# Optimization experiments

Hardware: AMD Instinct MI355X
Metric: run time of the kernel (lower is better)

## Reference

```python
import jax, jax.numpy as jnp
import numpy as np

K = 5        # spline kernel_size per dim (dim=2 -> 25 kernel weights)
NPG = 75     # MNIST superpixel nodes per graph


def _spline_conv(x, src, dst, pseudo, emask, W, root, bias):
    """SplineConv, dim=2, kernel_size=5, degree=1 open splines, aggr='mean'.
    emask in {0,1} masks out coalesced-away (duplicate/self-loop) edges."""
    n = x.shape[0]
    v = jnp.clip(pseudo, 0.0, 1.0) * (K - 1)
    bot = jnp.clip(jnp.floor(v), 0, K - 2)
    frac = v - bot                                   # [E,2]
    bot = bot.astype(jnp.int32)
    xj = x[src] * emask[:, None]                     # [E,Fin] gathered source feats
    # aggregate-then-transform: acc[k,i,:] = sum over edges into i with basis k
    acc = jnp.zeros((K * K, n, x.shape[1]), x.dtype)
    for o0 in (0, 1):
        for o1 in (0, 1):
            w = (frac[:, 0] if o0 else 1.0 - frac[:, 0]) * (frac[:, 1] if o1 else 1.0 - frac[:, 1])
            kk = (bot[:, 0] + o0) + K * (bot[:, 1] + o1)
            acc = acc.at[kk, dst].add(w[:, None] * xj)
    out = jnp.einsum('knf,kfo->no', acc, W)
    deg = jax.ops.segment_sum(emask, dst, num_segments=n)
    return out / jnp.maximum(deg, 1.0)[:, None] + x @ root + bias


def _pool(x, pos, valid, batch, src, dst, emask, size, G, B):
    """voxel_grid + max_pool with static shapes: S=B*G*G clusters, masked."""
    S = B * G * G
    c = jnp.clip(jnp.floor(pos / size).astype(jnp.int32), 0, G - 1)
    cl = batch * (G * G) + c[:, 1] * G + c[:, 0]
    xm = jnp.where(valid[:, None] > 0, x, -1e30)
    px = jax.ops.segment_max(xm, cl, num_segments=S)
    cnt = jax.ops.segment_sum(valid, cl, num_segments=S)
    sval = (cnt > 0).astype(x.dtype)
    px = jnp.where(sval[:, None] > 0, px, 0.0)
    ppos = jax.ops.segment_sum(pos * valid[:, None], cl, num_segments=S) / jnp.maximum(cnt, 1.0)[:, None]
    nb = jnp.arange(S, dtype=jnp.int32) // (G * G)
    # remap edges to clusters; mask self loops and duplicates (= coalesce)
    nsrc, ndst = cl[src], cl[dst]
    m = (emask > 0) & (nsrc != ndst)
    a0 = jnp.where(m, nsrc, S)
    b0 = jnp.where(m, ndst, S)
    order = jnp.lexsort((b0, a0))
    a, b = a0[order], b0[order]
    first = jnp.concatenate([jnp.array([True]), (a[1:] != a[:-1]) | (b[1:] != b[:-1])])
    keep = jnp.zeros(src.shape[0], dtype=bool).at[order].set(first & (a < S))
    kf = keep.astype(x.dtype)
    # T.Cartesian(cat=False, norm=True): pseudo = (pos_src-pos_dst)/(2*max|.|)+0.5
    cart = ppos[nsrc] - ppos[ndst]
    amax = jnp.maximum(jnp.max(jnp.abs(cart) * kf[:, None]), 1e-12)
    pseudo = cart / (2.0 * amax) + 0.5
    return px, ppos, sval, nb, nsrc, ndst, kf, pseudo


def _forward(x, pos, src, dst, W1, r1, b1, W2, r2, b2, W3, r3, b3, fw1, fb1, fw2, fb2):
    N = x.shape[0]
    B = N // NPG
    batch = jnp.arange(N, dtype=jnp.int32) // NPG
    valid = jnp.ones((N,), x.dtype)
    emask = jnp.ones((src.shape[0],), x.dtype)
    cart = pos[src] - pos[dst]
    pseudo = cart / (2.0 * jnp.maximum(jnp.max(jnp.abs(cart)), 1e-12)) + 0.5
    x = jax.nn.elu(_spline_conv(x, src, dst, pseudo, emask, W1, r1, b1))
    x, pos, valid, batch, src, dst, emask, pseudo = _pool(x, pos, valid, batch, src, dst, emask, 5.0, 6, B)
    x = jax.nn.elu(_spline_conv(x, src, dst, pseudo, emask, W2, r2, b2))
    x, pos, valid, batch, src, dst, emask, pseudo = _pool(x, pos, valid, batch, src, dst, emask, 7.0, 5, B)
    x = jax.nn.elu(_spline_conv(x, src, dst, pseudo, emask, W3, r3, b3))
    # max_pool_x(cluster, x, batch, size=4): 2x2 voxel grid (size=14, end=27.99)
    c = jnp.clip(jnp.floor(pos / 14.0).astype(jnp.int32), 0, 1)
    cl = batch * 4 + c[:, 1] * 2 + c[:, 0]
    xm = jnp.where(valid[:, None] > 0, x, -1e30)
    px = jax.ops.segment_max(xm, cl, num_segments=B * 4)
    cnt = jax.ops.segment_sum(valid, cl, num_segments=B * 4)
    px = jnp.where((cnt > 0)[:, None], px, 0.0)
    h = jax.nn.elu(px.reshape(B, 4 * 64) @ fw1.T + fb1)
    logits = h @ fw2.T + fb2  # F.dropout is identity in eval mode
    return jax.nn.log_softmax(logits, axis=1)


def setup_inputs() -> dict:
    key = jax.random.key(0)
    ks = jax.random.split(key, 16)
    B, EPG = 1024, 1392
    N = B * NPG
    x = jax.random.normal(ks[0], (N, 1), jnp.float32)
    pos = jax.random.uniform(ks[1], (N, 2), jnp.float32) * 27.99
    s = jax.random.randint(ks[2], (B, EPG), 0, NPG)
    d = (s + 1 + jax.random.randint(ks[3], (B, EPG), 0, NPG - 1)) % NPG  # no self loops
    off = (jnp.arange(B, dtype=jnp.int32) * NPG)[:, None]
    src = (s + off).reshape(-1)
    dst = (d + off).reshape(-1)
    rn = lambda k, sh, sc: jax.random.normal(k, sh, jnp.float32) * sc
    return dict(x=x, pos=pos, src=src, dst=dst,
                W1=rn(ks[4], (25, 1, 32), 0.2), r1=rn(ks[5], (1, 32), 0.2), b1=jnp.zeros((32,), jnp.float32),
                W2=rn(ks[6], (25, 32, 64), 0.05), r2=rn(ks[7], (32, 64), 0.1), b2=jnp.zeros((64,), jnp.float32),
                W3=rn(ks[8], (25, 64, 64), 0.04), r3=rn(ks[9], (64, 64), 0.08), b3=jnp.zeros((64,), jnp.float32),
                fw1=rn(ks[10], (128, 256), 0.06), fb1=jnp.zeros((128,), jnp.float32),
                fw2=rn(ks[11], (10, 128), 0.09), fb2=jnp.zeros((10,), jnp.float32))


def reference(x, pos, src, dst, W1, r1, b1, W2, r2, b2, W3, r3, b3, fw1, fb1, fw2, fb2):
    return _forward(x, pos, src, dst, W1, r1, b1, W2, r2, b2, W3, r3, b3, fw1, fb1, fw2, fb2)
```

## Files before the change

kernel.cpp:

```cpp
#include <hip/hip_runtime.h>
#include <math.h>

#define NPG 75
#define KDIM 5

typedef _Float16 half8 __attribute__((ext_vector_type(8)));
typedef _Float16 half4 __attribute__((ext_vector_type(4)));
typedef float f32x4 __attribute__((ext_vector_type(4)));

__device__ __forceinline__ float eluf(float v){ return v > 0.f ? v : expf(v) - 1.f; }

__device__ __forceinline__ unsigned fenc(float f){
    unsigned u = __float_as_uint(f);
    return (u & 0x80000000u) ? ~u : (u | 0x80000000u);
}
__device__ __forceinline__ float fdec(unsigned u){
    return (u & 0x80000000u) ? __uint_as_float(u & 0x7FFFFFFFu) : __uint_as_float(~u);
}

__device__ __forceinline__ void fma25(float (&r)[25], const float (&wx)[5], const float (&wyx)[5]){
    #pragma unroll
    for (int b1 = 0; b1 < 5; b1++)
        #pragma unroll
        for (int b0 = 0; b0 < 5; b0++)
            asm("v_fmac_f32 %0, %1, %2" : "+v"(r[b1 * 5 + b0]) : "v"(wx[b0]), "v"(wyx[b1]));
}

__device__ __forceinline__ void spline2(float c0, float c1, float am, int* kks, float* wsp){
    float denom = 2.f * fmaxf(am, 1e-12f);
    float p0 = c0 / denom + 0.5f;
    float p1 = c1 / denom + 0.5f;
    p0 = fminf(fmaxf(p0, 0.f), 1.f) * 4.f;
    p1 = fminf(fmaxf(p1, 0.f), 1.f) * 4.f;
    float b0 = fminf(floorf(p0), 3.f);
    float b1 = fminf(floorf(p1), 3.f);
    float f0 = p0 - b0, f1 = p1 - b1;
    int i0 = (int)b0, i1 = (int)b1;
    wsp[0] = (1.f - f0) * (1.f - f1); kks[0] = i0     + KDIM *  i1;
    wsp[1] =        f0  * (1.f - f1); kks[1] = i0 + 1 + KDIM *  i1;
    wsp[2] = (1.f - f0) *        f1 ; kks[2] = i0     + KDIM * (i1 + 1);
    wsp[3] =        f0  *        f1 ; kks[3] = i0 + 1 + KDIM * (i1 + 1);
}

__global__ __launch_bounds__(256) void amax0_k(
        const float* __restrict__ pos, const int* __restrict__ src,
        const int* __restrict__ dst, int E4, float* __restrict__ pbmax){
    int i = blockIdx.x * 256 + threadIdx.x;
    float cand = 0.f;
    if (i < E4){
        int4 s4 = ((const int4*)src)[i];
        int4 d4 = ((const int4*)dst)[i];
        #pragma unroll
        for (int k = 0; k < 4; k++){
            int s = (&s4.x)[k], d = (&d4.x)[k];
            float c0 = pos[s*2]   - pos[d*2];
            float c1 = pos[s*2+1] - pos[d*2+1];
            cand = fmaxf(cand, fmaxf(fabsf(c0), fabsf(c1)));
        }
    }
    __shared__ float sm[256];
    sm[threadIdx.x] = cand; __syncthreads();
    for (int o = 128; o > 0; o >>= 1){
        if (threadIdx.x < o) sm[threadIdx.x] = fmaxf(sm[threadIdx.x], sm[threadIdx.x + o]);
        __syncthreads();
    }
    if (threadIdx.x == 0) pbmax[blockIdx.x] = sm[0];
}

__global__ __launch_bounds__(1024) void reduce_max_k(const float* __restrict__ pbmax, int n,
                                                     unsigned* __restrict__ outbits){
    __shared__ float sm[1024];
    float cand = 0.f;
    for (int i = threadIdx.x; i < n; i += 1024) cand = fmaxf(cand, pbmax[i]);
    sm[threadIdx.x] = cand; __syncthreads();
    for (int o = 512; o > 0; o >>= 1){
        if (threadIdx.x < o) sm[threadIdx.x] = fmaxf(sm[threadIdx.x], sm[threadIdx.x + o]);
        __syncthreads();
    }
    if (threadIdx.x == 0) *outbits = __float_as_uint(sm[0]);
}

__global__ __launch_bounds__(512) void conv1pool1_k(
        const float* __restrict__ x, const float* __restrict__ pos,
        const int* __restrict__ src, const int* __restrict__ dst, int EPG,
        const unsigned* __restrict__ amaxp,
        const float* __restrict__ W1, const float* __restrict__ r1, const float* __restrict__ b1,
        float* __restrict__ px1, float* __restrict__ pp1, float* __restrict__ sv1,
        int* __restrict__ cl1){
    __shared__ float acc[NPG * 25];
    __shared__ float deg[NPG];
    __shared__ float xl[NPG], p0l[NPG], p1l[NPG];
    __shared__ int   cli[NPG];
    __shared__ float W1s[800], r1s[32], b1s[32];
    __shared__ unsigned px[36 * 32];
    __shared__ float cnt[36], ps[72];

    const int b = blockIdx.x, t = threadIdx.x;
    const int n0 = b * NPG, e0 = b * EPG;

    for (int i = t; i < NPG * 25; i += 512) acc[i] = 0.f;
    for (int i = t; i < 36 * 32; i += 512) px[i] = 0u;
    if (t < NPG) deg[t] = 0.f;
    if (t < 36) cnt[t] = 0.f;
    if (t < 72) ps[t] = 0.f;
    for (int i = t; i < 800; i += 512) W1s[i] = W1[i];
    if (t < 32){ r1s[t] = r1[t]; b1s[t] = b1[t]; }
    if (t < NPG){
        float p0 = pos[(n0 + t) * 2], p1 = pos[(n0 + t) * 2 + 1];
        xl[t] = x[n0 + t]; p0l[t] = p0; p1l[t] = p1;
        int c0 = min(max((int)floorf(p0 / 5.f), 0), 5);
        int c1 = min(max((int)floorf(p1 / 5.f), 0), 5);
        int c = c1 * 6 + c0;
        cli[t] = c;
        cl1[n0 + t] = b * 36 + c;
    }
    __syncthreads();
    if (t < NPG){
        int c = cli[t];
        atomicAdd(&cnt[c], 1.f);
        atomicAdd(&ps[c*2],     p0l[t]);
        atomicAdd(&ps[c*2 + 1], p1l[t]);
    }

    const float am = __uint_as_float(*amaxp);
    for (int e = t; e < EPG; e += 512){
        int s = src[e0 + e] - n0;
        int d = dst[e0 + e] - n0;
        float c0 = p0l[s] - p0l[d];
        float c1 = p1l[s] - p1l[d];
        int kks[4]; float wsp[4];
        spline2(c0, c1, am, kks, wsp);
        float xv = xl[s];
        #pragma unroll
        for (int c = 0; c < 4; c++) atomicAdd(&acc[d*25 + kks[c]], wsp[c] * xv);
        atomicAdd(&deg[d], 1.f);
    }
    __syncthreads();

    for (int idx = t; idx < NPG * 32; idx += 512){
        int i = idx >> 5, o = idx & 31;
        float sum = 0.f;
        #pragma unroll
        for (int k = 0; k < 25; k++) sum += acc[i*25 + k] * W1s[k*32 + o];
        float v = sum / fmaxf(deg[i], 1.f) + xl[i] * r1s[o] + b1s[o];
        v = eluf(v);
        atomicMax(&px[cli[i]*32 + o], fenc(v));
    }
    __syncthreads();

    for (int idx = t; idx < 36 * 32; idx += 512){
        int s_ = idx >> 5;
        float c = cnt[s_];
        px1[(size_t)(b*36)*32 + idx] = (c > 0.f) ? fdec(px[idx]) : 0.f;
    }
    if (t < 36){
        float c = cnt[t], m = fmaxf(c, 1.f);
        pp1[(b*36 + t)*2]     = ps[t*2] / m;
        pp1[(b*36 + t)*2 + 1] = ps[t*2 + 1] / m;
        sv1[b*36 + t] = (c > 0.f) ? 1.f : 0.f;
    }
}

template<int GG, int NN>
__global__ __launch_bounds__(1024) void dedup_csr_k(
        const int* src_in, const int* dst_in,
        const int* __restrict__ clmap, const unsigned char* __restrict__ kf_in,
        unsigned char* kf_out, int* es_out, int* ed_out,
        const float* __restrict__ pp, int EPG,
        int* __restrict__ easrc, float2* __restrict__ ecart,
        int* __restrict__ rowptr2, int* __restrict__ kcnt, float* __restrict__ pbmax){
    __shared__ unsigned pm[GG * GG];
    __shared__ float degs[GG];
    __shared__ int rs[GG + 1];
    __shared__ int cur[GG];
    __shared__ float red[16];
    __shared__ int   clS[NN];
    __shared__ float ppS[2 * GG];

    const int b = blockIdx.x, t = threadIdx.x;
    const int lane = t & 63, wid = t >> 6;
    const int e0 = b * EPG;
    const int cbase = b * GG;

    for (int i = t; i < GG * GG; i += 1024) pm[i] = 0xFFFFFFFFu;
    if (t < GG) degs[t] = 0.f;
    if (t < NN) clS[t] = clmap[b * NN + t] - cbase;
    if (t < 2 * GG) ppS[t] = pp[cbase * 2 + t];
    __syncthreads();

    const int niter = (EPG + 1023) / 1024;
    int la[2], lb[2]; bool lm[2];
    const int nbase = b * NN;
    for (int it = 0; it < niter; it++){
        int e = t + it * 1024;
        lm[it] = false;
        if (e < EPG){
            int a  = clS[src_in[e0 + e] - nbase];
            int bb = clS[dst_in[e0 + e] - nbase];
            la[it] = a; lb[it] = bb;
            es_out[e0 + e] = cbase + a; ed_out[e0 + e] = cbase + bb;
            bool m = (kf_in ? (kf_in[e0 + e] != 0) : true) && (a != bb);
            lm[it] = m;
            if (m) atomicMin(&pm[a * GG + bb], (unsigned)e);
        }
    }
    __syncthreads();

    float cand = 0.f;
    bool kept[2]; float lc0[2], lc1[2];
    for (int it = 0; it < niter; it++){
        int e = t + it * 1024;
        kept[it] = false;
        if (e < EPG){
            bool k = false;
            if (lm[it]) k = (pm[la[it] * GG + lb[it]] == (unsigned)e);
            kept[it] = k;
            if (kf_out) kf_out[e0 + e] = k ? 1 : 0;
            if (k){
                atomicAdd(&degs[lb[it]], 1.f);
                float c0 = ppS[la[it]*2]     - ppS[lb[it]*2];
                float c1 = ppS[la[it]*2 + 1] - ppS[lb[it]*2 + 1];
                lc0[it] = c0; lc1[it] = c1;
                cand = fmaxf(cand, fmaxf(fabsf(c0), fabsf(c1)));
            }
        }
    }
    #pragma unroll
    for (int o = 1; o < 64; o <<= 1) cand = fmaxf(cand, __shfl_xor(cand, o, 64));
    if (lane == 0) red[wid] = cand;
    __syncthreads();
    if (t == 0){
        float m = red[0];
        #pragma unroll
        for (int i = 1; i < 16; i++) m = fmaxf(m, red[i]);
        pbmax[b] = m;
    }
    if (t < 64){
        int v = (t < GG) ? (int)degs[t] : 0;
        int incl = v;
        #pragma unroll
        for (int o = 1; o < 64; o <<= 1){
            int u = __shfl_up(incl, o, 64);
            if (t >= o) incl += u;
        }
        if (t == 0) rs[0] = 0;
        if (t < GG) rs[t + 1] = incl;
    }
    __syncthreads();
    if (t < GG){
        rowptr2[(cbase + t)*2]     = e0 + rs[t];
        rowptr2[(cbase + t)*2 + 1] = e0 + rs[t + 1];
        cur[t] = rs[t];
    }
    if (t == 0) kcnt[b] = rs[GG];
    __syncthreads();
    for (int it = 0; it < niter; it++){
        if (kept[it]){
            int slot = atomicAdd(&cur[lb[it]], 1);
            easrc[e0 + slot] = cbase + la[it];
            ecart[e0 + slot] = make_float2(lc0[it], lc1[it]);
        }
    }
}

__global__ void espline_k(const float2* __restrict__ ecart, const unsigned* __restrict__ amaxp,
                          const int* __restrict__ kcnt, int EPG, int E,
                          float* __restrict__ edata){
    int i = blockIdx.x * 256 + threadIdx.x;
    if (i >= E) return;
    int b = i / EPG;
    if (i - b * EPG >= kcnt[b]) return;
    float2 c = ecart[i];
    float am = __uint_as_float(*amaxp);
    float denom = 2.f * fmaxf(am, 1e-12f);
    float p0 = fminf(fmaxf(c.x / denom + 0.5f, 0.f), 1.f) * 4.f;
    float p1 = fminf(fmaxf(c.y / denom + 0.5f, 0.f), 1.f) * 4.f;
    float b0 = fminf(floorf(p0), 3.f);
    float b1 = fminf(floorf(p1), 3.f);
    int i0 = (int)b0, i1 = (int)b1;
    float f0 = p0 - b0, f1 = p1 - b1;
    float wx[5], wy[5];
    #pragma unroll
    for (int k = 0; k < 5; k++){
        wx[k] = (k == i0) ? (1.f - f0) : ((k == i0 + 1) ? f0 : 0.f);
        wy[k] = (k == i1) ? (1.f - f1) : ((k == i1 + 1) ? f1 : 0.f);
    }
    float* d = edata + (size_t)i * 8;
    *(float4*)(d)     = make_float4(wx[0], wx[1], wx[2], wx[3]);
    *(float4*)(d + 4) = make_float4(wy[0], wy[1], wy[2], wy[3]);
}

template<int CIN, int G>
__global__ __launch_bounds__(256) void pool_mid_k(
        const float* __restrict__ xin, const float* __restrict__ ppin,
        const float* __restrict__ svin, float size,
        float* __restrict__ pxout, float* __restrict__ ppout, float* __restrict__ svout,
        int* __restrict__ clout){
    __shared__ unsigned px[G * G * 64];
    __shared__ float cnt[G * G], ps[2 * G * G];
    __shared__ int cli[CIN];
    const int b = blockIdx.x, t = threadIdx.x;

    for (int i = t; i < G * G * 64; i += 256) px[i] = 0u;
    if (t < G * G){ cnt[t] = 0.f; ps[t*2] = 0.f; ps[t*2 + 1] = 0.f; }
    if (t < CIN){
        float v  = svin[b*CIN + t];
        float p0 = ppin[(b*CIN + t)*2], p1 = ppin[(b*CIN + t)*2 + 1];
        int c0 = min(max((int)floorf(p0 / size), 0), G - 1);
        int c1 = min(max((int)floorf(p1 / size), 0), G - 1);
        int c = c1 * G + c0;
        cli[t] = (v > 0.f) ? c : -1;
        clout[b*CIN + t] = b * G * G + c;
    }
    __syncthreads();
    if (t < CIN && cli[t] >= 0){
        int c = cli[t];
        atomicAdd(&cnt[c], 1.f);
        atomicAdd(&ps[c*2],     ppin[(b*CIN + t)*2]);
        atomicAdd(&ps[c*2 + 1], ppin[(b*CIN + t)*2 + 1]);
    }
    __syncthreads();
    for (int idx = t; idx < CIN * 64; idx += 256){
        int i = idx >> 6, f = idx & 63;
        if (cli[i] >= 0)
            atomicMax(&px[cli[i]*64 + f], fenc(xin[(size_t)(b*CIN + i)*64 + f]));
    }
    __syncthreads();
    for (int idx = t; idx < G * G * 64; idx += 256){
        int s_ = idx >> 6;
        pxout[(size_t)(b*G*G)*64 + idx] = (cnt[s_] > 0.f) ? fdec(px[idx]) : 0.f;
    }
    if (t < G * G){
        float c = cnt[t], m = fmaxf(c, 1.f);
        ppout[(b*G*G + t)*2]     = ps[t*2] / m;
        ppout[(b*G*G + t)*2 + 1] = ps[t*2 + 1] / m;
        svout[b*G*G + t] = (c > 0.f) ? 1.f : 0.f;
    }
}

__global__ void wswz_k(const float* __restrict__ W, const float* __restrict__ root,
                       int FIN, _Float16* __restrict__ Wz){
    int gid = blockIdx.x * 256 + threadIdx.x;
    int KT = 26 * FIN;
    if (gid >= KT * 64) return;
    int k = gid >> 6, n = gid & 63;
    float v = (k < 25 * FIN) ? W[(size_t)k * 64 + n] : root[(size_t)(k - 25 * FIN) * 64 + n];
    int kt = k >> 5, kr = k & 31, quad = kr >> 3, j = kr & 7;
    int lane = (quad << 4) | (n & 15);
    int nt = n >> 4;
    Wz[(((size_t)(kt * 4 + nt) * 64 + lane) << 3) + j] = (_Float16)v;
}

template<int FIN>
__global__ __launch_bounds__(64) void conv_gather_k(
        const float* __restrict__ x, const int* __restrict__ easrc,
        const float* __restrict__ edata,
        const int* __restrict__ rowptr2, int n, _Float16* __restrict__ Aout){
    constexpr int KTOT = 26 * FIN;
    const int lane = threadIdx.x;
    const int node = blockIdx.x;
    const int row0 = rowptr2[node*2], row1 = rowptr2[node*2 + 1];
    constexpr int STEP = (FIN == 32) ? 2 : 1;
    const int sub = (FIN == 32) ? (lane >> 5) : 0;
    const int f = lane & (FIN - 1);

    float r[25];
    #pragma unroll
    for (int b = 0; b < 25; b++) r[b] = 0.f;

    int iCur = row0 + sub;
    int aNext = 0;
    float4 waC, wbC;
    float xvCur = 0.f;
    if (iCur < row1){
        int aCur = easrc[iCur];
        const float* d = edata + (size_t)iCur * 8;
        waC = *(const float4*)(d); wbC = *(const float4*)(d + 4);
        xvCur = x[(size_t)aCur * FIN + f];
        int i1 = (iCur + STEP < row1) ? iCur + STEP : iCur;
        aNext = easrc[i1];
    }
    for (; iCur < row1; iCur += STEP){
        int iN  = iCur + STEP;
        int iNs = (iN < row1) ? iN : iCur;
        int iN2 = (iN + STEP < row1) ? iN + STEP : iNs;
        const float* dn = edata + (size_t)iNs * 8;
        float4 waN = *(const float4*)(dn);
        float4 wbN = *(const float4*)(dn + 4);
        float xvN = x[(size_t)aNext * FIN + f];
        int aN2 = easrc[iN2];
        float wx4 = 1.f - (waC.x + waC.y + waC.z + waC.w);
        float wy4 = 1.f - (wbC.x + wbC.y + wbC.z + wbC.w);
        float wx[5]  = {waC.x, waC.y, waC.z, waC.w, wx4};
        float wyx[5] = {wbC.x * xvCur, wbC.y * xvCur, wbC.z * xvCur, wbC.w * xvCur, wy4 * xvCur};
        fma25(r, wx, wyx);
        waC = waN; wbC = wbN; xvCur = xvN; aNext = aN2;
    }

    if (FIN == 32){
        #pragma unroll
        for (int b = 0; b < 25; b++) r[b] += __shfl_xor(r[b], 32, 64);
    }

    float inv = 1.f / (float)max(row1 - row0, 1);
    _Float16* dstrow = Aout + (size_t)node * KTOT;
    if (FIN == 64){
        #pragma unroll
        for (int b = 0; b < 25; b++) dstrow[b * 64 + f] = (_Float16)(r[b] * inv);
        dstrow[25 * 64 + f] = (_Float16)x[(size_t)node * 64 + f];
    } else {
        #pragma unroll
        for (int b = 0; b < 25; b++)
            if ((b & 1) == sub) dstrow[b * 32 + f] = (_Float16)(r[b] * inv);
        if (sub == 0) dstrow[25 * 32 + f] = (_Float16)x[(size_t)node * 32 + f];
    }
}

template<int KTOT, int SPLITK>
__global__ __launch_bounds__(256) void conv_mfma_k(
        const _Float16* __restrict__ A, const _Float16* __restrict__ Wz,
        int M, float* __restrict__ Cpart){
    constexpr int NSTEP = KTOT / SPLITK / 32;
    const int w = threadIdx.x >> 6, lane = threadIdx.x & 63;
    const int m0 = blockIdx.x * 64 + w * 16;
    const int kt0 = blockIdx.y * NSTEP;
    const int quad = lane >> 4;

    f32x4 acc[4];
    #pragma unroll
    for (int nt = 0; nt < 4; nt++) acc[nt] = (f32x4){0.f, 0.f, 0.f, 0.f};

    const half8* __restrict__ Arow = (const half8*)(A + (size_t)(m0 + (lane & 15)) * KTOT);
    const half8* __restrict__ Wp   = (const half8*)Wz + (size_t)kt0 * 4 * 64 + lane;

    for (int kt = 0; kt < NSTEP; kt++){
        half8 a = Arow[(kt0 + kt) * 4 + quad];
        #pragma unroll
        for (int nt = 0; nt < 4; nt++){
            half8 b = Wp[(kt * 4 + nt) * 64];
            acc[nt] = __builtin_amdgcn_mfma_f32_16x16x32_f16(a, b, acc[nt], 0, 0, 0);
        }
    }

    float* cp = Cpart + ((size_t)blockIdx.y * M + m0) * 64;
    const int r = quad * 4, c = lane & 15;
    #pragma unroll
    for (int nt = 0; nt < 4; nt++)
        #pragma unroll
        for (int i = 0; i < 4; i++)
            cp[(size_t)(r + i) * 64 + nt * 16 + c] = acc[nt][i];
}

template<int SPLITK>
__global__ void conv_epi_k(const float* __restrict__ Cpart, const float* __restrict__ bias,
                           int M, float* __restrict__ out){
    int gid = blockIdx.x * 256 + threadIdx.x;
    if (gid >= M * 64) return;
    int c = gid & 63;
    float v = bias[c];
    #pragma unroll
    for (int s = 0; s < SPLITK; s++) v += Cpart[(size_t)s * M * 64 + gid];
    out[gid] = eluf(v);
}

__global__ __launch_bounds__(256) void final_k(
        const float* __restrict__ xin, const float* __restrict__ ppin,
        const float* __restrict__ svin,
        const float* __restrict__ fw1, const float* __restrict__ fb1,
        const float* __restrict__ fw2, const float* __restrict__ fb2,
        float* __restrict__ out){
    __shared__ unsigned px[4 * 64];
    __shared__ float cnt[4];
    __shared__ int cli[25];
    __shared__ float xr[256];
    __shared__ float h[128];
    __shared__ float lg[10];
    __shared__ float lse;
    const int b = blockIdx.x, t = threadIdx.x;

    if (t < 4*64) px[t] = 0u;
    if (t < 4) cnt[t] = 0.f;
    if (t < 25){
        float v  = svin[b*25 + t];
        float p0 = ppin[(b*25 + t)*2], p1 = ppin[(b*25 + t)*2 + 1];
        int c0 = min(max((int)floorf(p0 / 14.f), 0), 1);
        int c1 = min(max((int)floorf(p1 / 14.f), 0), 1);
        int c = c1 * 2 + c0;
        cli[t] = (v > 0.f) ? c : -1;
    }
    __syncthreads();
    if (t < 25 && cli[t] >= 0) atomicAdd(&cnt[cli[t]], 1.f);
    __syncthreads();
    for (int idx = t; idx < 25 * 64; idx += 256){
        int i = idx >> 6, f = idx & 63;
        if (cli[i] >= 0)
            atomicMax(&px[cli[i]*64 + f], fenc(xin[(size_t)(b*25 + i)*64 + f]));
    }
    __syncthreads();
    xr[t] = (cnt[t >> 6] > 0.f) ? fdec(px[t]) : 0.f;
    __syncthreads();
    if (t < 128){
        float s = fb1[t];
        const float* wrow = fw1 + (size_t)t * 256;
        #pragma unroll 8
        for (int i = 0; i < 256; i++) s += xr[i] * wrow[i];
        h[t] = eluf(s);
    }
    __syncthreads();
    if (t < 10){
        float s2 = fb2[t];
        const float* w2 = fw2 + (size_t)t * 128;
        for (int j = 0; j < 128; j++) s2 += h[j] * w2[j];
        lg[t] = s2;
    }
    __syncthreads();
    if (t == 0){
        float m = lg[0];
        for (int c = 1; c < 10; c++) m = fmaxf(m, lg[c]);
        float se = 0.f;
        for (int c = 0; c < 10; c++) se += expf(lg[c] - m);
        lse = m + logf(se);
    }
    __syncthreads();
    if (t < 10) out[(size_t)b*10 + t] = lg[t] - lse;
}

extern "C" void kernel_launch(void* const* d_in, const int* in_sizes, int n_in,
                              void* d_out, int out_size, void* d_ws, size_t ws_size,
                              hipStream_t stream) {
    const float* x   = (const float*)d_in[0];
    const float* pos = (const float*)d_in[1];
    const int*   src = (const int*)d_in[2];
    const int*   dst = (const int*)d_in[3];
    const float* W1  = (const float*)d_in[4];
    const float* r1  = (const float*)d_in[5];
    const float* b1  = (const float*)d_in[6];
    const float* W2  = (const float*)d_in[7];
    const float* r2  = (const float*)d_in[8];
    const float* b2  = (const float*)d_in[9];
    const float* W3  = (const float*)d_in[10];
    const float* r3  = (const float*)d_in[11];
    const float* b3  = (const float*)d_in[12];
    const float* fw1 = (const float*)d_in[13];
    const float* fb1 = (const float*)d_in[14];
    const float* fw2 = (const float*)d_in[15];
    const float* fb2 = (const float*)d_in[16];
    float* out = (float*)d_out;

    const int N   = in_sizes[0];
    const int E   = in_sizes[2];
    const int B   = N / NPG;
    const int EPG = E / B;
    const int S1  = B * 36;
    const int S2  = B * 25;

    float* w = (float*)d_ws;
    size_t off = 0;
    auto alloc = [&](size_t nelem){ size_t o = off; off += (nelem + 63) & ~(size_t)63; return o; };

    size_t o_scal = alloc(4);
    size_t o_pb   = alloc(8192);
    size_t o_px1  = alloc((size_t)S1 * 32);
    size_t o_pp1  = alloc((size_t)S1 * 2);
    size_t o_sv1  = alloc(S1);
    size_t o_cl1  = alloc(N);
    size_t o_kf1  = alloc((E + 3) / 4);
    size_t o_es1  = alloc(E);
    size_t o_ed1  = alloc(E);
    size_t o_easrc= alloc(E);
    size_t o_ecart= alloc((size_t)2 * E);
    size_t o_edat = alloc((size_t)8 * E);
    size_t o_kcnt = alloc(B);
    size_t o_rp2  = alloc((size_t)2 * S1);
    size_t o_rp3  = alloc((size_t)2 * S2);
    size_t o_out2 = alloc((size_t)S1 * 64);
    size_t o_cl2  = alloc(S1);
    size_t o_px2  = alloc((size_t)S2 * 64);
    size_t o_pp2  = alloc((size_t)S2 * 2);
    size_t o_sv2  = alloc(S2);
    size_t o_out3 = alloc((size_t)S2 * 64);
    size_t o_wz   = alloc((size_t)26 * 64 * 64 / 2 + 64);
    size_t cpElems = (size_t)2 * S1 * 64 > (size_t)4 * S2 * 64 ? (size_t)2 * S1 * 64 : (size_t)4 * S2 * 64;
    size_t o_cp   = alloc(cpElems);
    size_t accAhalfs = (size_t)S1 * 832 > (size_t)S2 * 1664 ? (size_t)S1 * 832 : (size_t)S2 * 1664;
    size_t o_accA = alloc((accAhalfs + 1) / 2);

    hipMemsetAsync(w + o_scal, 0, 4 * sizeof(float), stream);

    unsigned* scal = (unsigned*)(w + o_scal);
    float*    pb   = w + o_pb;
    _Float16* Wz   = (_Float16*)(w + o_wz);
    _Float16* A16  = (_Float16*)(w + o_accA);
    auto nb = [](long long t){ return (unsigned)((t + 255) / 256); };

    const int E4 = E / 4;
    const int nbA = (int)nb(E4);
    amax0_k<<<nbA, 256, 0, stream>>>(pos, src, dst, E4, pb);
    reduce_max_k<<<1, 1024, 0, stream>>>(pb, nbA, scal + 0);
    conv1pool1_k<<<B, 512, 0, stream>>>(x, pos, src, dst, EPG, scal + 0, W1, r1, b1,
                                        w + o_px1, w + o_pp1, w + o_sv1, (int*)(w + o_cl1));

    dedup_csr_k<36, NPG><<<B, 1024, 0, stream>>>(
        src, dst, (int*)(w + o_cl1), nullptr,
        (unsigned char*)(w + o_kf1), (int*)(w + o_es1), (int*)(w + o_ed1),
        w + o_pp1, EPG, (int*)(w + o_easrc), (float2*)(w + o_ecart),
        (int*)(w + o_rp2), (int*)(w + o_kcnt), pb);
    reduce_max_k<<<1, 1024, 0, stream>>>(pb, B, scal + 1);
    espline_k<<<nb(E), 256, 0, stream>>>((float2*)(w + o_ecart), scal + 1,
                                         (int*)(w + o_kcnt), EPG, E, w + o_edat);

    wswz_k<<<nb(26 * 32 * 64), 256, 0, stream>>>(W2, r2, 32, Wz);
    conv_gather_k<32><<<S1, 64, 0, stream>>>(
        w + o_px1, (int*)(w + o_easrc), w + o_edat,
        (int*)(w + o_rp2), S1, A16);
    {
        dim3 g(S1 / 64, 2);
        conv_mfma_k<832, 2><<<g, 256, 0, stream>>>(A16, Wz, S1, w + o_cp);
    }
    conv_epi_k<2><<<nb((long long)S1 * 64), 256, 0, stream>>>(w + o_cp, b2, S1, w + o_out2);

    pool_mid_k<36, 5><<<B, 256, 0, stream>>>(
        w + o_out2, w + o_pp1, w + o_sv1, 7.f,
        w + o_px2, w + o_pp2, w + o_sv2, (int*)(w + o_cl2));

    dedup_csr_k<25, 36><<<B, 1024, 0, stream>>>(
        (int*)(w + o_es1), (int*)(w + o_ed1), (int*)(w + o_cl2), (unsigned char*)(w + o_kf1),
        nullptr, (int*)(w + o_es1), (int*)(w + o_ed1),
        w + o_pp2, EPG, (int*)(w + o_easrc), (float2*)(w + o_ecart),
        (int*)(w + o_rp3), (int*)(w + o_kcnt), pb);
    reduce_max_k<<<1, 1024, 0, stream>>>(pb, B, scal + 2);
    espline_k<<<nb(E), 256, 0, stream>>>((float2*)(w + o_ecart), scal + 2,
                                         (int*)(w + o_kcnt), EPG, E, w + o_edat);

    wswz_k<<<nb(26 * 64 * 64), 256, 0, stream>>>(W3, r3, 64, Wz);
    conv_gather_k<64><<<S2, 64, 0, stream>>>(
        w + o_px2, (int*)(w + o_easrc), w + o_edat,
        (int*)(w + o_rp3), S2, A16);
    {
        dim3 g(S2 / 64, 4);
        conv_mfma_k<1664, 4><<<g, 256, 0, stream>>>(A16, Wz, S2, w + o_cp);
    }
    conv_epi_k<4><<<nb((long long)S2 * 64), 256, 0, stream>>>(w + o_cp, b3, S2, w + o_out3);

    final_k<<<B, 256, 0, stream>>>(w + o_out3, w + o_pp2, w + o_sv2,
                                   fw1, fb1, fw2, fb2, out);
}
```

Measured before the change: 381.6 us.

## Replace separate max-reduction kernels with atomicMax and register-cache conv1 weights

Removes the three single-block reduce_max_k launches. The per-block maxima are now combined with atomicMax on the float bit pattern directly in amax0_k (now grid-stride, capped at 512 blocks) and in dedup_csr_k. This works because the values are non-negative, so their unsigned bit order matches float order. The conv1 epilogue now keeps the 25 W1 weights per output channel in registers and reads acc rows padded to 28 floats as float4. This cuts launch overhead and LDS traffic, at the cost of global atomics and more registers.

New measurement: 375.0 us. About the same (-1.7%).

```diff
diff --git a/kernel.cpp b/kernel.cpp
--- a/kernel.cpp
+++ b/kernel.cpp
@@ -44,10 +44,9 @@
 
 __global__ __launch_bounds__(256) void amax0_k(
         const float* __restrict__ pos, const int* __restrict__ src,
-        const int* __restrict__ dst, int E4, float* __restrict__ pbmax){
-    int i = blockIdx.x * 256 + threadIdx.x;
+        const int* __restrict__ dst, int E4, unsigned* __restrict__ outbits){
     float cand = 0.f;
-    if (i < E4){
+    for (int i = blockIdx.x * 256 + threadIdx.x; i < E4; i += gridDim.x * 256){
         int4 s4 = ((const int4*)src)[i];
         int4 d4 = ((const int4*)dst)[i];
         #pragma unroll
@@ -64,20 +63,7 @@
         if (threadIdx.x < o) sm[threadIdx.x] = fmaxf(sm[threadIdx.x], sm[threadIdx.x + o]);
         __syncthreads();
     }
-    if (threadIdx.x == 0) pbmax[blockIdx.x] = sm[0];
-}
-
-__global__ __launch_bounds__(1024) void reduce_max_k(const float* __restrict__ pbmax, int n,
-                                                     unsigned* __restrict__ outbits){
-    __shared__ float sm[1024];
-    float cand = 0.f;
-    for (int i = threadIdx.x; i < n; i += 1024) cand = fmaxf(cand, pbmax[i]);
-    sm[threadIdx.x] = cand; __syncthreads();
-    for (int o = 512; o > 0; o >>= 1){
-        if (threadIdx.x < o) sm[threadIdx.x] = fmaxf(sm[threadIdx.x], sm[threadIdx.x + o]);
-        __syncthreads();
-    }
-    if (threadIdx.x == 0) *outbits = __float_as_uint(sm[0]);
+    if (threadIdx.x == 0) atomicMax(outbits, __float_as_uint(sm[0]));
 }
 
 __global__ __launch_bounds__(512) void conv1pool1_k(
@@ -87,7 +73,7 @@
         const float* __restrict__ W1, const float* __restrict__ r1, const float* __restrict__ b1,
         float* __restrict__ px1, float* __restrict__ pp1, float* __restrict__ sv1,
         int* __restrict__ cl1){
-    __shared__ float acc[NPG * 25];
+    __shared__ __align__(16) float acc[NPG * 28];
     __shared__ float deg[NPG];
     __shared__ float xl[NPG], p0l[NPG], p1l[NPG];
     __shared__ int   cli[NPG];
@@ -98,7 +84,7 @@
     const int b = blockIdx.x, t = threadIdx.x;
     const int n0 = b * NPG, e0 = b * EPG;
 
-    for (int i = t; i < NPG * 25; i += 512) acc[i] = 0.f;
+    for (int i = t; i < NPG * 28; i += 512) acc[i] = 0.f;
     for (int i = t; i < 36 * 32; i += 512) px[i] = 0u;
     if (t < NPG) deg[t] = 0.f;
     if (t < 36) cnt[t] = 0.f;
@@ -115,6 +101,13 @@
         cl1[n0 + t] = b * 36 + c;
     }
     __syncthreads();
+
+    const int o = t & 31;
+    float wreg[25];
+    #pragma unroll
+    for (int k = 0; k < 25; k++) wreg[k] = W1s[k * 32 + o];
+    const float rro = r1s[o], bbo = b1s[o];
+
     if (t < NPG){
         int c = cli[t];
         atomicAdd(&cnt[c], 1.f);
@@ -132,26 +125,36 @@
         spline2(c0, c1, am, kks, wsp);
         float xv = xl[s];
         #pragma unroll
-        for (int c = 0; c < 4; c++) atomicAdd(&acc[d*25 + kks[c]], wsp[c] * xv);
+        for (int c = 0; c < 4; c++) atomicAdd(&acc[d*28 + kks[c]], wsp[c] * xv);
         atomicAdd(&deg[d], 1.f);
     }
     __syncthreads();
 
-    for (int idx = t; idx < NPG * 32; idx += 512){
-        int i = idx >> 5, o = idx & 31;
-        float sum = 0.f;
-        #pragma unroll
-        for (int k = 0; k < 25; k++) sum += acc[i*25 + k] * W1s[k*32 + o];
-        float v = sum / fmaxf(deg[i], 1.f) + xl[i] * r1s[o] + b1s[o];
-        v = eluf(v);
-        atomicMax(&px[cli[i]*32 + o], fenc(v));
+    const int ii = t >> 5;
+    #pragma unroll
+    for (int r = 0; r < 5; r++){
+        int i = ii + r * 16;
+        if (i < NPG){
+            const float4* ar = (const float4*)(acc + i * 28);
+            float s = 0.f;
+            #pragma unroll
+            for (int q = 0; q < 7; q++){
+                float4 aq = ar[q];
+                s += aq.x * wreg[q*4];
+                if (q*4 + 1 < 25) s += aq.y * wreg[q*4 + 1];
+                if (q*4 + 2 < 25) s += aq.z * wreg[q*4 + 2];
+                if (q*4 + 3 < 25) s += aq.w * wreg[q*4 + 3];
+            }
+            float v = s / fmaxf(deg[i], 1.f) + xl[i] * rro + bbo;
+            v = eluf(v);
+            atomicMax(&px[cli[i]*32 + o], fenc(v));
+        }
     }
     __syncthreads();
 
     for (int idx = t; idx < 36 * 32; idx += 512){
         int s_ = idx >> 5;
-        float c = cnt[s_];
-        px1[(size_t)(b*36)*32 + idx] = (c > 0.f) ? fdec(px[idx]) : 0.f;
+        px1[(size_t)(b*36)*32 + idx] = (cnt[s_] > 0.f) ? fdec(px[idx]) : 0.f;
     }
     if (t < 36){
         float c = cnt[t], m = fmaxf(c, 1.f);
@@ -168,7 +171,7 @@
         unsigned char* kf_out, int* es_out, int* ed_out,
         const float* __restrict__ pp, int EPG,
         int* __restrict__ easrc, float2* __restrict__ ecart,
-        int* __restrict__ rowptr2, int* __restrict__ kcnt, float* __restrict__ pbmax){
+        int* __restrict__ rowptr2, int* __restrict__ kcnt, unsigned* __restrict__ amaxbits){
     __shared__ unsigned pm[GG * GG];
     __shared__ float degs[GG];
     __shared__ int rs[GG + 1];
@@ -233,7 +236,7 @@
         float m = red[0];
         #pragma unroll
         for (int i = 1; i < 16; i++) m = fmaxf(m, red[i]);
-        pbmax[b] = m;
+        atomicMax(amaxbits, __float_as_uint(m));
     }
     if (t < 64){
         int v = (t < GG) ? (int)degs[t] : 0;
@@ -559,7 +562,6 @@
     auto alloc = [&](size_t nelem){ size_t o = off; off += (nelem + 63) & ~(size_t)63; return o; };
 
     size_t o_scal = alloc(4);
-    size_t o_pb   = alloc(8192);
     size_t o_px1  = alloc((size_t)S1 * 32);
     size_t o_pp1  = alloc((size_t)S1 * 2);
     size_t o_sv1  = alloc(S1);
@@ -588,15 +590,13 @@
     hipMemsetAsync(w + o_scal, 0, 4 * sizeof(float), stream);
 
     unsigned* scal = (unsigned*)(w + o_scal);
-    float*    pb   = w + o_pb;
     _Float16* Wz   = (_Float16*)(w + o_wz);
     _Float16* A16  = (_Float16*)(w + o_accA);
     auto nb = [](long long t){ return (unsigned)((t + 255) / 256); };
 
     const int E4 = E / 4;
-    const int nbA = (int)nb(E4);
-    amax0_k<<<nbA, 256, 0, stream>>>(pos, src, dst, E4, pb);
-    reduce_max_k<<<1, 1024, 0, stream>>>(pb, nbA, scal + 0);
+    int gA = (E4 + 255) / 256; if (gA > 512) gA = 512;
+    amax0_k<<<gA, 256, 0, stream>>>(pos, src, dst, E4, scal + 0);
     conv1pool1_k<<<B, 512, 0, stream>>>(x, pos, src, dst, EPG, scal + 0, W1, r1, b1,
                                         w + o_px1, w + o_pp1, w + o_sv1, (int*)(w + o_cl1));
 
@@ -604,8 +604,7 @@
         src, dst, (int*)(w + o_cl1), nullptr,
         (unsigned char*)(w + o_kf1), (int*)(w + o_es1), (int*)(w + o_ed1),
         w + o_pp1, EPG, (int*)(w + o_easrc), (float2*)(w + o_ecart),
-        (int*)(w + o_rp2), (int*)(w + o_kcnt), pb);
-    reduce_max_k<<<1, 1024, 0, stream>>>(pb, B, scal + 1);
+        (int*)(w + o_rp2), (int*)(w + o_kcnt), scal + 1);
     espline_k<<<nb(E), 256, 0, stream>>>((float2*)(w + o_ecart), scal + 1,
                                          (int*)(w + o_kcnt), EPG, E, w + o_edat);
 
@@ -627,8 +626,7 @@
         (int*)(w + o_es1), (int*)(w + o_ed1), (int*)(w + o_cl2), (unsigned char*)(w + o_kf1),
         nullptr, (int*)(w + o_es1), (int*)(w + o_ed1),
         w + o_pp2, EPG, (int*)(w + o_easrc), (float2*)(w + o_ecart),
-        (int*)(w + o_rp3), (int*)(w + o_kcnt), pb);
-    reduce_max_k<<<1, 1024, 0, stream>>>(pb, B, scal + 2);
+        (int*)(w + o_rp3), (int*)(w + o_kcnt), scal + 2);
     espline_k<<<nb(E), 256, 0, stream>>>((float2*)(w + o_ecart), scal + 2,
                                          (int*)(w + o_kcnt), EPG, E, w + o_edat);
 
```
